# Kernel optimization log

Hardware: AMD Instinct MI355X
Metric: run time of the kernel (lower is better)

The kernel has to match this reference:

```python
import jax, jax.numpy as jnp
import numpy as np

N_VERT = 100000
N_EDGE = 50000
NNZ = 3200000
IN_CH = 256
OUT_CH = 64


def setup_inputs() -> dict:
    key = jax.random.key(0)
    k1, k2, k3, k4, k5, k6 = jax.random.split(key, 6)
    X = jax.random.normal(k1, (N_VERT, IN_CH), dtype=jnp.float32)
    W = jax.random.normal(k2, (OUT_CH, IN_CH), dtype=jnp.float32) * (IN_CH ** -0.5)
    degE = jax.random.uniform(k3, (N_EDGE,), dtype=jnp.float32, minval=0.01, maxval=1.0)
    degV = jax.random.uniform(k4, (N_VERT,), dtype=jnp.float32, minval=0.01, maxval=1.0)
    Wdiag = jnp.ones((N_EDGE,), dtype=jnp.float32)
    v_idx = jax.random.randint(k5, (NNZ,), 0, N_VERT, dtype=jnp.int32)
    e_idx = jax.random.randint(k6, (NNZ,), 0, N_EDGE, dtype=jnp.int32)
    return {"X": X, "W": W, "degE": degE, "degV": degV, "Wdiag": Wdiag,
            "v_idx": v_idx, "e_idx": e_idx}


def reference(X, W, degE, degV, Wdiag, v_idx, e_idx):
    # Dense projection: [N, in] @ [in, out] -> [N, out]
    Xp = jnp.einsum('ni,oi->no', X, W)
    # Stage 1: vertex -> hyperedge aggregation, degE + Wdiag normalization
    Xe = jax.ops.segment_sum(Xp[v_idx], e_idx, num_segments=N_EDGE)
    Xe = Xe * (degE * Wdiag)[:, None]
    # Stage 2: hyperedge -> vertex aggregation, degV normalization
    Xv = jax.ops.segment_sum(Xe[e_idx], v_idx, num_segments=N_VERT)
    Xv = Xv * degV[:, None]
    return Xv
```

## Files before the change

kernel.cpp:

```cpp
#include <hip/hip_runtime.h>

#define NV   100000
#define NE   50000
#define NNZ  3200000
#define KIN  256
#define KOUT 64

#define NB    128
#define CHUNK (NNZ / NB)
#define NBE   782
#define NBV   1563
#define NBINS (NBE + NBV)
#define LSCAN (NBINS * NB)
#define NBLK_SCAN ((LSCAN + 1023) / 1024)

#define ECAP_E 6144
#define ECAP_V 4096

typedef short short8 __attribute__((ext_vector_type(8)));
typedef float f32x4  __attribute__((ext_vector_type(4)));

__device__ __forceinline__ unsigned short f2bf(float f) {
    union { float f; unsigned u; } c{f};
    const unsigned lsb = (c.u >> 16) & 1u;
    return (unsigned short)((c.u + 0x7FFFu + lsb) >> 16);
}
__device__ __forceinline__ float bf2f_lo(unsigned u) {
    union { unsigned u; float f; } c{u << 16};
    return c.f;
}
__device__ __forceinline__ float bf2f_hi(unsigned u) {
    union { unsigned u; float f; } c{u & 0xFFFF0000u};
    return c.f;
}
__device__ __forceinline__ short8 pack8(const float4 lo, const float4 hi) {
    short8 r;
    r[0] = (short)f2bf(lo.x); r[1] = (short)f2bf(lo.y);
    r[2] = (short)f2bf(lo.z); r[3] = (short)f2bf(lo.w);
    r[4] = (short)f2bf(hi.x); r[5] = (short)f2bf(hi.y);
    r[6] = (short)f2bf(hi.z); r[7] = (short)f2bf(hi.w);
    return r;
}

__global__ __launch_bounds__(256) void k_wb(const float* __restrict__ W,
                                            unsigned short* __restrict__ Wb) {
    const int i = blockIdx.x * 256 + threadIdx.x;
    Wb[i] = f2bf(W[i]);
}

__global__ __launch_bounds__(256) void k_project(const float* __restrict__ X,
                                                 const unsigned short* __restrict__ Wb,
                                                 unsigned short* __restrict__ Xpb) {
    const int tid  = threadIdx.x;
    const int lane = tid & 63;
    const int wv   = tid >> 6;
    const int l15  = lane & 15;
    const int l4   = lane >> 4;
    const int rbase = blockIdx.x * 128 + wv * 32;

    const int r0 = min(rbase + l15,      NV - 1);
    const int r1 = min(rbase + 16 + l15, NV - 1);
    const float* xp0 = X + (size_t)r0 * KIN + l4 * 8;
    const float* xp1 = X + (size_t)r1 * KIN + l4 * 8;
    const unsigned short* wp = Wb + (size_t)l15 * KIN + l4 * 8;

    f32x4 acc[2][4];
#pragma unroll
    for (int t = 0; t < 2; ++t)
#pragma unroll
        for (int g = 0; g < 4; ++g)
            acc[t][g] = (f32x4){0.f, 0.f, 0.f, 0.f};

#pragma unroll
    for (int s = 0; s < 8; ++s) {
        const int k0 = s * 32;
        const float4 a0lo = *(const float4*)(xp0 + k0);
        const float4 a0hi = *(const float4*)(xp0 + k0 + 4);
        const float4 a1lo = *(const float4*)(xp1 + k0);
        const float4 a1hi = *(const float4*)(xp1 + k0 + 4);
        short8 b[4];
#pragma unroll
        for (int g = 0; g < 4; ++g)
            b[g] = *(const short8*)(wp + (size_t)g * 16 * KIN + k0);
        const short8 a0 = pack8(a0lo, a0hi);
        const short8 a1 = pack8(a1lo, a1hi);
#pragma unroll
        for (int g = 0; g < 4; ++g) {
            acc[0][g] = __builtin_amdgcn_mfma_f32_16x16x32_bf16(a0, b[g], acc[0][g], 0, 0, 0);
            acc[1][g] = __builtin_amdgcn_mfma_f32_16x16x32_bf16(a1, b[g], acc[1][g], 0, 0, 0);
        }
    }

#pragma unroll
    for (int t = 0; t < 2; ++t)
#pragma unroll
        for (int i = 0; i < 4; ++i) {
            const int r = rbase + t * 16 + l4 * 4 + i;
            if (r < NV) {
#pragma unroll
                for (int g = 0; g < 4; ++g)
                    Xpb[(size_t)r * KOUT + g * 16 + l15] = f2bf(acc[t][g][i]);
            }
        }
}

__global__ __launch_bounds__(1024) void k_hist(const int* __restrict__ v_idx,
                                               const int* __restrict__ e_idx,
                                               int* __restrict__ mat) {
    __shared__ int h[NBINS];
    const int b = blockIdx.x, tid = threadIdx.x;
    for (int i = tid; i < NBINS; i += 1024) h[i] = 0;
    __syncthreads();
    const int base = b * CHUNK;
    for (int i = tid; i < CHUNK; i += 1024) {
        atomicAdd(&h[e_idx[base + i] >> 6], 1);
        atomicAdd(&h[NBE + (v_idx[base + i] >> 6)], 1);
    }
    __syncthreads();
    for (int j = tid; j < NBINS; j += 1024) mat[j * NB + b] = h[j];
}

__global__ __launch_bounds__(1024) void k_scan1(int* __restrict__ mat,
                                                int* __restrict__ bsum) {
    __shared__ int buf[1024];
    const int tid = threadIdx.x;
    const int i = blockIdx.x * 1024 + tid;
    const int v = (i < LSCAN) ? mat[i] : 0;
    buf[tid] = v;
    __syncthreads();
    for (int d = 1; d < 1024; d <<= 1) {
        int t = (tid >= d) ? buf[tid - d] : 0;
        __syncthreads();
        buf[tid] += t;
        __syncthreads();
    }
    if (i < LSCAN) mat[i] = buf[tid] - v;
    if (tid == 1023) bsum[blockIdx.x] = buf[1023];
}

__global__ __launch_bounds__(1024) void k_scan2(int* __restrict__ bsum) {
    __shared__ int buf[1024];
    const int tid = threadIdx.x;
    const int v = (tid < NBLK_SCAN) ? bsum[tid] : 0;
    buf[tid] = v;
    __syncthreads();
    for (int d = 1; d < 1024; d <<= 1) {
        int t = (tid >= d) ? buf[tid - d] : 0;
        __syncthreads();
        buf[tid] += t;
        __syncthreads();
    }
    if (tid < NBLK_SCAN) bsum[tid] = buf[tid] - v;
}

__global__ __launch_bounds__(1024) void k_scan3(int* __restrict__ mat,
                                                const int* __restrict__ bsum) {
    const int i = blockIdx.x * 1024 + threadIdx.x;
    if (i < LSCAN) mat[i] += bsum[blockIdx.x];
}

__global__ __launch_bounds__(1024) void k_partition2(const int* __restrict__ v_idx,
                                                     const int* __restrict__ e_idx,
                                                     const int* __restrict__ mat,
                                                     unsigned* __restrict__ partE,
                                                     unsigned* __restrict__ partV) {
    __shared__ int curE[NBE];
    __shared__ int curV[NBV];
    const int b = blockIdx.x, tid = threadIdx.x;
    for (int j = tid; j < NBE; j += 1024) curE[j] = mat[j * NB + b];
    for (int j = tid; j < NBV; j += 1024) curV[j] = mat[(NBE + j) * NB + b] - NNZ;
    __syncthreads();
    const int base = b * CHUNK;
    for (int i = tid; i < CHUNK; i += 1024) {
        const int v = v_idx[base + i];
        const int e = e_idx[base + i];
        const int pE = atomicAdd(&curE[e >> 6], 1);
        partE[pE] = (unsigned)v | ((unsigned)(e & 63) << 17);
        const int pV = atomicAdd(&curV[v >> 6], 1);
        partV[pV] = (unsigned)e | ((unsigned)(v & 63) << 17);
    }
}

__global__ __launch_bounds__(1024) void k_sortgatherE(const unsigned* __restrict__ part,
                                                      const int* __restrict__ mat,
                                                      const unsigned short* __restrict__ Xpb,
                                                      const float* __restrict__ degE,
                                                      const float* __restrict__ Wdiag,
                                                      unsigned short* __restrict__ Xeb) {
    __shared__ unsigned sbuf[ECAP_E];
    __shared__ int hist[64], cur[64], pfx[65];
    const int b = blockIdx.x, tid = threadIdx.x;
    const int base = mat[b * NB];
    const int end  = (b == NBE - 1) ? NNZ : mat[(b + 1) * NB];
    const int nb = end - base;

    if (tid < 64) hist[tid] = 0;
    __syncthreads();
    for (int i = tid; i < nb; i += 1024)
        atomicAdd(&hist[(part[base + i] >> 17) & 63], 1);
    __syncthreads();
    if (tid == 0) {
        int s = 0;
        for (int k = 0; k < 64; ++k) { pfx[k] = s; cur[k] = s; s += hist[k]; }
        pfx[64] = s;
    }
    __syncthreads();
    for (int i = tid; i < nb; i += 1024) {
        const unsigned u = part[base + i];
        const int p = atomicAdd(&cur[(u >> 17) & 63], 1);
        sbuf[p] = u & 0x1FFFFu;
    }
    __syncthreads();

    const int wv = tid >> 6, lane = tid & 63;
    const int q = lane >> 3, sl = lane & 7;
#pragma unroll
    for (int j = 0; j < 4; ++j) {
        const int le = wv * 4 + j;
        const int e_id = (b << 6) + le;
        const int s0 = pfx[le];
        const int n  = pfx[le + 1] - s0;
        float a0 = 0.f, a1 = 0.f, a2 = 0.f, a3 = 0.f,
              a4 = 0.f, a5 = 0.f, a6 = 0.f, a7 = 0.f;
        const int nf = n >> 3;
        int t = 0;
        for (; t + 4 <= nf; t += 4) {
            int idx[4]; uint4 u4[4];
#pragma unroll
            for (int z = 0; z < 4; ++z) idx[z] = (int)sbuf[s0 + 8 * (t + z) + q];
#pragma unroll
            for (int z = 0; z < 4; ++z)
                u4[z] = *(const uint4*)&Xpb[(size_t)idx[z] * KOUT + 8 * sl];
#pragma unroll
            for (int z = 0; z < 4; ++z) {
                a0 += bf2f_lo(u4[z].x); a1 += bf2f_hi(u4[z].x);
                a2 += bf2f_lo(u4[z].y); a3 += bf2f_hi(u4[z].y);
                a4 += bf2f_lo(u4[z].z); a5 += bf2f_hi(u4[z].z);
                a6 += bf2f_lo(u4[z].w); a7 += bf2f_hi(u4[z].w);
            }
        }
        for (; t < nf; ++t) {
            const int idx = (int)sbuf[s0 + 8 * t + q];
            const uint4 u = *(const uint4*)&Xpb[(size_t)idx * KOUT + 8 * sl];
            a0 += bf2f_lo(u.x); a1 += bf2f_hi(u.x);
            a2 += bf2f_lo(u.y); a3 += bf2f_hi(u.y);
            a4 += bf2f_lo(u.z); a5 += bf2f_hi(u.z);
            a6 += bf2f_lo(u.w); a7 += bf2f_hi(u.w);
        }
        if (n & 7) {
            const int src = nf * 8 + q;
            if (src < n) {
                const int idx = (int)sbuf[s0 + src];
                const uint4 u = *(const uint4*)&Xpb[(size_t)idx * KOUT + 8 * sl];
                a0 += bf2f_lo(u.x); a1 += bf2f_hi(u.x);
                a2 += bf2f_lo(u.y); a3 += bf2f_hi(u.y);
                a4 += bf2f_lo(u.z); a5 += bf2f_hi(u.z);
                a6 += bf2f_lo(u.w); a7 += bf2f_hi(u.w);
            }
        }
#pragma unroll
        for (int d = 8; d < 64; d <<= 1) {
            a0 += __shfl_xor(a0, d, 64); a1 += __shfl_xor(a1, d, 64);
            a2 += __shfl_xor(a2, d, 64); a3 += __shfl_xor(a3, d, 64);
            a4 += __shfl_xor(a4, d, 64); a5 += __shfl_xor(a5, d, 64);
            a6 += __shfl_xor(a6, d, 64); a7 += __shfl_xor(a7, d, 64);
        }
        if (q == 0 && e_id < NE) {
            const float s = degE[e_id] * Wdiag[e_id];
            uint4 pk;
            pk.x = (unsigned)f2bf(a0 * s) | ((unsigned)f2bf(a1 * s) << 16);
            pk.y = (unsigned)f2bf(a2 * s) | ((unsigned)f2bf(a3 * s) << 16);
            pk.z = (unsigned)f2bf(a4 * s) | ((unsigned)f2bf(a5 * s) << 16);
            pk.w = (unsigned)f2bf(a6 * s) | ((unsigned)f2bf(a7 * s) << 16);
            *(uint4*)&Xeb[(size_t)e_id * KOUT + 8 * sl] = pk;
        }
    }
}

__global__ __launch_bounds__(1024) void k_sortgatherV(const unsigned* __restrict__ part,
                                                      const int* __restrict__ mat,
                                                      const unsigned short* __restrict__ Xeb,
                                                      const float* __restrict__ degV,
                                                      float* __restrict__ out) {
    __shared__ unsigned sbuf[ECAP_V];
    __shared__ int hist[64], cur[64], pfx[65];
    const int b = blockIdx.x, tid = threadIdx.x;
    const int base = mat[NBE * NB + b * NB] - NNZ;
    const int end  = (b == NBV - 1) ? NNZ : (mat[NBE * NB + (b + 1) * NB] - NNZ);
    const int nb = end - base;

    if (tid < 64) hist[tid] = 0;
    __syncthreads();
    for (int i = tid; i < nb; i += 1024)
        atomicAdd(&hist[(part[base + i] >> 17) & 63], 1);
    __syncthreads();
    if (tid == 0) {
        int s = 0;
        for (int k = 0; k < 64; ++k) { pfx[k] = s; cur[k] = s; s += hist[k]; }
        pfx[64] = s;
    }
    __syncthreads();
    for (int i = tid; i < nb; i += 1024) {
        const unsigned u = part[base + i];
        const int p = atomicAdd(&cur[(u >> 17) & 63], 1);
        sbuf[p] = u & 0x1FFFFu;
    }
    __syncthreads();

    const int wv = tid >> 6, lane = tid & 63;
    const int q = lane >> 3, sl = lane & 7;
#pragma unroll
    for (int j = 0; j < 4; ++j) {
        const int lv = wv * 4 + j;
        const int v_id = (b << 6) + lv;
        const int s0 = pfx[lv];
        const int n  = pfx[lv + 1] - s0;
        float a0 = 0.f, a1 = 0.f, a2 = 0.f, a3 = 0.f,
              a4 = 0.f, a5 = 0.f, a6 = 0.f, a7 = 0.f;
        const int nf = n >> 3;
        int t = 0;
        for (; t + 4 <= nf; t += 4) {
            int idx[4]; uint4 u4[4];
#pragma unroll
            for (int z = 0; z < 4; ++z) idx[z] = (int)sbuf[s0 + 8 * (t + z) + q];
#pragma unroll
            for (int z = 0; z < 4; ++z)
                u4[z] = *(const uint4*)&Xeb[(size_t)idx[z] * KOUT + 8 * sl];
#pragma unroll
            for (int z = 0; z < 4; ++z) {
                a0 += bf2f_lo(u4[z].x); a1 += bf2f_hi(u4[z].x);
                a2 += bf2f_lo(u4[z].y); a3 += bf2f_hi(u4[z].y);
                a4 += bf2f_lo(u4[z].z); a5 += bf2f_hi(u4[z].z);
                a6 += bf2f_lo(u4[z].w); a7 += bf2f_hi(u4[z].w);
            }
        }
        for (; t < nf; ++t) {
            const int idx = (int)sbuf[s0 + 8 * t + q];
            const uint4 u = *(const uint4*)&Xeb[(size_t)idx * KOUT + 8 * sl];
            a0 += bf2f_lo(u.x); a1 += bf2f_hi(u.x);
            a2 += bf2f_lo(u.y); a3 += bf2f_hi(u.y);
            a4 += bf2f_lo(u.z); a5 += bf2f_hi(u.z);
            a6 += bf2f_lo(u.w); a7 += bf2f_hi(u.w);
        }
        if (n & 7) {
            const int src = nf * 8 + q;
            if (src < n) {
                const int idx = (int)sbuf[s0 + src];
                const uint4 u = *(const uint4*)&Xeb[(size_t)idx * KOUT + 8 * sl];
                a0 += bf2f_lo(u.x); a1 += bf2f_hi(u.x);
                a2 += bf2f_lo(u.y); a3 += bf2f_hi(u.y);
                a4 += bf2f_lo(u.z); a5 += bf2f_hi(u.z);
                a6 += bf2f_lo(u.w); a7 += bf2f_hi(u.w);
            }
        }
#pragma unroll
        for (int d = 8; d < 64; d <<= 1) {
            a0 += __shfl_xor(a0, d, 64); a1 += __shfl_xor(a1, d, 64);
            a2 += __shfl_xor(a2, d, 64); a3 += __shfl_xor(a3, d, 64);
            a4 += __shfl_xor(a4, d, 64); a5 += __shfl_xor(a5, d, 64);
            a6 += __shfl_xor(a6, d, 64); a7 += __shfl_xor(a7, d, 64);
        }
        if (q == 0 && v_id < NV) {
            const float s = degV[v_id];
            *(float4*)&out[(size_t)v_id * KOUT + 8 * sl] =
                make_float4(a0 * s, a1 * s, a2 * s, a3 * s);
            *(float4*)&out[(size_t)v_id * KOUT + 8 * sl + 4] =
                make_float4(a4 * s, a5 * s, a6 * s, a7 * s);
        }
    }
}

extern "C" void kernel_launch(void* const* d_in, const int* in_sizes, int n_in,
                              void* d_out, int out_size, void* d_ws, size_t ws_size,
                              hipStream_t stream) {
    const float* X     = (const float*)d_in[0];
    const float* W     = (const float*)d_in[1];
    const float* degE  = (const float*)d_in[2];
    const float* degV  = (const float*)d_in[3];
    const float* Wdiag = (const float*)d_in[4];
    const int*   v_idx = (const int*)d_in[5];
    const int*   e_idx = (const int*)d_in[6];
    float* out = (float*)d_out;

    unsigned short* Xpb  = (unsigned short*)d_ws;
    unsigned short* Xeb  = Xpb + (size_t)NV * KOUT;
    unsigned*       partE = (unsigned*)(Xeb + (size_t)NE * KOUT);
    unsigned*       partV = partE + NNZ;
    int*            mat   = (int*)(partV + NNZ);
    int*            bsum  = mat + LSCAN;
    unsigned short* Wb    = (unsigned short*)(bsum + ((NBLK_SCAN + 3) & ~3));

    k_wb<<<(KIN * KOUT) / 256, 256, 0, stream>>>(W, Wb);
    k_project<<<(NV + 127) / 128, 256, 0, stream>>>(X, Wb, Xpb);

    k_hist<<<NB, 1024, 0, stream>>>(v_idx, e_idx, mat);
    k_scan1<<<NBLK_SCAN, 1024, 0, stream>>>(mat, bsum);
    k_scan2<<<1, 1024, 0, stream>>>(bsum);
    k_scan3<<<NBLK_SCAN, 1024, 0, stream>>>(mat, bsum);

    k_partition2<<<NB, 1024, 0, stream>>>(v_idx, e_idx, mat, partE, partV);

    k_sortgatherE<<<NBE, 1024, 0, stream>>>(partE, mat, Xpb, degE, Wdiag, Xeb);
    k_sortgatherV<<<NBV, 1024, 0, stream>>>(partV, mat, Xeb, degV, out);
}
```

Baseline: 238.7 us.

## Replace scattered partition with tiled local-sort partition per side

The single partition kernel, which scattered each element directly to global memory via shared-memory bin counters, is replaced by two kernels, one for edge bins and one for vertex bins. Each block now sorts 6250-element tiles locally in LDS by bin, then writes them out so that entries of the same bin go to contiguous global addresses. The block count doubles to 256, which also changes the histogram and scan layout sizes. This aims to coalesce scattered global writes, at the cost of reading the indices twice, extra synchronisation and more LDS use per block.

Result: faster. 226.0 us, median of 2 (-5.3%).

```diff
diff --git a/kernel.cpp b/kernel.cpp
--- a/kernel.cpp
+++ b/kernel.cpp
@@ -6,8 +6,9 @@
 #define KIN  256
 #define KOUT 64
 
-#define NB    128
+#define NB    256
 #define CHUNK (NNZ / NB)
+#define TS    6250
 #define NBE   782
 #define NBV   1563
 #define NBINS (NBE + NBV)
@@ -159,25 +160,79 @@
     if (i < LSCAN) mat[i] += bsum[blockIdx.x];
 }
 
-__global__ __launch_bounds__(1024) void k_partition2(const int* __restrict__ v_idx,
-                                                     const int* __restrict__ e_idx,
-                                                     const int* __restrict__ mat,
-                                                     unsigned* __restrict__ partE,
-                                                     unsigned* __restrict__ partV) {
-    __shared__ int curE[NBE];
-    __shared__ int curV[NBV];
+template <int SIDE, int NBIN>
+__global__ __launch_bounds__(1024) void k_partsort(const int* __restrict__ v_idx,
+                                                   const int* __restrict__ e_idx,
+                                                   const int* __restrict__ mat,
+                                                   unsigned* __restrict__ part) {
+    __shared__ unsigned sbuf[TS];
+    __shared__ unsigned short binbuf[TS];
+    __shared__ int hist[NBIN], pfx[NBIN], cur[NBIN], gdst[NBIN];
     const int b = blockIdx.x, tid = threadIdx.x;
-    for (int j = tid; j < NBE; j += 1024) curE[j] = mat[j * NB + b];
-    for (int j = tid; j < NBV; j += 1024) curV[j] = mat[(NBE + j) * NB + b] - NNZ;
-    __syncthreads();
+    const int rowOff = SIDE ? NBE : 0;
+    const int sub    = SIDE ? NNZ : 0;
+
+    for (int j = tid; j < NBIN; j += 1024)
+        gdst[j] = mat[(rowOff + j) * NB + b] - sub;
+
     const int base = b * CHUNK;
-    for (int i = tid; i < CHUNK; i += 1024) {
-        const int v = v_idx[base + i];
-        const int e = e_idx[base + i];
-        const int pE = atomicAdd(&curE[e >> 6], 1);
-        partE[pE] = (unsigned)v | ((unsigned)(e & 63) << 17);
-        const int pV = atomicAdd(&curV[v >> 6], 1);
-        partV[pV] = (unsigned)e | ((unsigned)(v & 63) << 17);
+    for (int tile = 0; tile < CHUNK / TS; ++tile) {
+        __syncthreads();
+        for (int j = tid; j < NBIN; j += 1024) hist[j] = 0;
+        __syncthreads();
+
+        int sb[7]; unsigned svv[7];
+#pragma unroll
+        for (int s = 0; s < 7; ++s) {
+            const int li = s * 1024 + tid;
+            sb[s] = -1;
+            if (li < TS) {
+                const int i = base + tile * TS + li;
+                const int v = v_idx[i], e = e_idx[i];
+                int bin; unsigned val;
+                if (SIDE == 0) { bin = e >> 6; val = (unsigned)v | ((unsigned)(e & 63) << 17); }
+                else           { bin = v >> 6; val = (unsigned)e | ((unsigned)(v & 63) << 17); }
+                atomicAdd(&hist[bin], 1);
+                sb[s] = bin; svv[s] = val;
+            }
+        }
+        __syncthreads();
+
+        if (tid < 64) {
+            int carry = 0;
+            for (int c = 0; c < NBIN; c += 64) {
+                const int j = c + tid;
+                const int h = (j < NBIN) ? hist[j] : 0;
+                int x = h;
+#pragma unroll
+                for (int d = 1; d < 64; d <<= 1) {
+                    const int y = __shfl_up(x, d, 64);
+                    if (tid >= d) x += y;
+                }
+                if (j < NBIN) pfx[j] = carry + x - h;
+                carry += __shfl(x, 63, 64);
+            }
+        }
+        __syncthreads();
+        for (int j = tid; j < NBIN; j += 1024) cur[j] = pfx[j];
+        __syncthreads();
+
+#pragma unroll
+        for (int s = 0; s < 7; ++s) {
+            if (sb[s] >= 0) {
+                const int p = atomicAdd(&cur[sb[s]], 1);
+                sbuf[p] = svv[s];
+                binbuf[p] = (unsigned short)sb[s];
+            }
+        }
+        __syncthreads();
+
+        for (int li = tid; li < TS; li += 1024) {
+            const int bin = binbuf[li];
+            part[gdst[bin] + (li - pfx[bin])] = sbuf[li];
+        }
+        __syncthreads();
+        for (int j = tid; j < NBIN; j += 1024) gdst[j] += cur[j] - pfx[j];
     }
 }
 
@@ -398,7 +453,8 @@
     k_scan2<<<1, 1024, 0, stream>>>(bsum);
     k_scan3<<<NBLK_SCAN, 1024, 0, stream>>>(mat, bsum);
 
-    k_partition2<<<NB, 1024, 0, stream>>>(v_idx, e_idx, mat, partE, partV);
+    k_partsort<0, NBE><<<NB, 1024, 0, stream>>>(v_idx, e_idx, mat, partE);
+    k_partsort<1, NBV><<<NB, 1024, 0, stream>>>(v_idx, e_idx, mat, partV);
 
     k_sortgatherE<<<NBE, 1024, 0, stream>>>(partE, mat, Xpb, degE, Wdiag, Xeb);
     k_sortgatherV<<<NBV, 1024, 0, stream>>>(partV, mat, Xeb, degV, out);
```
